# Kernel tuning notes

Hardware: AMD Instinct MI355X
Metric: run time of the kernel (lower is better)

Reference implementation:

```python
import jax, jax.numpy as jnp
import numpy as np

# Geometry constants hardcoded in the torch module
B, H, W = 1, 256, 256
A, DC = 64, 1024            # n_views, det_count
NSAMP = 512                  # samples per ray for the line integral
DSRC, DDET, SPACING = 500.0, 500.0, 2.0
NPAD = 2048                  # fft padding (next pow2 >= 2*DC)
FEAT = 32


def _bilinear_image(img, px, py):
    """Bilinear sample img (B,H,W) at centered coords px,py (any shape). Zero outside."""
    b, hh, ww = img.shape
    cx = px + (ww - 1) / 2.0
    cy = py + (hh - 1) / 2.0
    x0 = jnp.floor(cx); y0 = jnp.floor(cy)
    fx = cx - x0; fy = cy - y0
    x0i = x0.astype(jnp.int32); y0i = y0.astype(jnp.int32)
    flat = img.reshape(b, -1)

    def gather(yi, xi):
        valid = (yi >= 0) & (yi < hh) & (xi >= 0) & (xi < ww)
        yc = jnp.clip(yi, 0, hh - 1); xc = jnp.clip(xi, 0, ww - 1)
        idx = (yc * ww + xc).reshape(-1)
        v = jnp.take(flat, idx, axis=1).reshape((b,) + yi.shape)
        return v * valid.astype(img.dtype)

    return (gather(y0i, x0i) * (1 - fx) * (1 - fy)
            + gather(y0i, x0i + 1) * fx * (1 - fy)
            + gather(y0i + 1, x0i) * (1 - fx) * fy
            + gather(y0i + 1, x0i + 1) * fx * fy)


def fan_forward(img, theta):
    """Ray-driven fan-beam forward projection. img (B,1,H,W) -> sino (B,A,DC)."""
    im = img[:, 0]
    c = jnp.cos(theta); s = jnp.sin(theta)
    src = DSRC * jnp.stack([c, s], -1)                    # (A,2) source positions
    e = jnp.stack([-s, c], -1)                            # detector axis
    u = (jnp.arange(DC) - (DC - 1) / 2.0) * SPACING       # detector offsets
    det = -DDET * jnp.stack([c, s], -1)[:, None, :] + u[None, :, None] * e[:, None, :]  # (A,DC,2)
    d = det - src[:, None, :]
    L = jnp.sqrt(jnp.sum(d * d, axis=-1))                 # (A,DC) ray lengths
    t = (jnp.arange(NSAMP, dtype=jnp.float32) + 0.5) / NSAMP
    pts = src[:, None, None, :] + t[None, None, :, None] * d[:, :, None, :]  # (A,DC,N,2)
    vals = _bilinear_image(im, pts[..., 0], pts[..., 1])  # (B,A,DC,N)
    return jnp.sum(vals, axis=-1) * (L / NSAMP)[None]


def filter_sinogram(sino):
    """Ram-Lak ramp filtering along the detector axis with zero-padding."""
    f = jnp.abs(jnp.fft.rfftfreq(NPAD)).astype(jnp.float32)  # cycles/sample
    sf = jnp.fft.rfft(sino, n=NPAD, axis=-1) * (2.0 * f)
    return jnp.fft.irfft(sf, n=NPAD, axis=-1)[..., :DC].astype(sino.dtype)


def fan_backprojection(sino, theta):
    """Pixel-driven fan-beam backprojection. sino (B,A,DC) -> (B,1,H,W)."""
    xs = jnp.arange(W, dtype=jnp.float32) - (W - 1) / 2.0
    ys = jnp.arange(H, dtype=jnp.float32) - (H - 1) / 2.0
    gx, gy = jnp.meshgrid(xs, ys)                         # (H,W)
    c = jnp.cos(theta)[:, None, None]; s = jnp.sin(theta)[:, None, None]
    xr = gx[None] * c + gy[None] * s                      # (A,H,W) rotated coords
    yr = -gx[None] * s + gy[None] * c
    denom = DSRC - xr
    uu = yr * (DSRC + DDET) / denom                       # detector coordinate
    wgt = (DSRC * DSRC) / (denom * denom)                 # fan-beam distance weight
    iu = uu / SPACING + (DC - 1) / 2.0
    i0 = jnp.floor(iu); fr = iu - i0
    i0i = i0.astype(jnp.int32)
    aidx = jnp.arange(A)[:, None, None]
    b = sino.shape[0]
    flat = sino.reshape(b, -1)

    def g(ii):
        valid = (ii >= 0) & (ii < DC)
        ic = jnp.clip(ii, 0, DC - 1)
        idx = (aidx * DC + ic).reshape(-1)
        v = jnp.take(flat, idx, axis=1).reshape((b, A, H, W))
        return v * valid.astype(sino.dtype)

    vals = g(i0i) * (1 - fr) + g(i0i + 1) * fr            # (B,A,H,W)
    bp = jnp.sum(vals * wgt[None], axis=1) * (jnp.pi / A)
    return bp[:, None]


def conv(x, w):
    return jax.lax.conv_general_dilated(x, w, (1, 1), 'SAME',
                                        dimension_numbers=('NCHW', 'OIHW', 'NCHW'))


def setup_inputs():
    key = jax.random.key(0)
    ks = jax.random.split(key, 8)
    x = jax.random.normal(ks[0], (B, 1, H, W), jnp.float32)
    theta = jnp.arange(A, dtype=jnp.float32) * (2.0 * np.pi / A)
    sinogram = jax.random.normal(ks[1], (B, A, DC), jnp.float32)

    def xav(k, shape):
        fan_in = shape[1] * 9; fan_out = shape[0] * 9
        return jax.random.normal(k, shape, jnp.float32) * np.sqrt(2.0 / (fan_in + fan_out)).astype(np.float32)

    return {
        'x': x, 'theta': theta, 'sinogram': sinogram,
        'lambda_step': jnp.float32(0.5), 'soft_thr': jnp.float32(0.01),
        'conv1_forward': xav(ks[2], (FEAT, 1, 3, 3)),
        'conv2_forward': xav(ks[3], (FEAT, FEAT, 3, 3)),
        'conv1_backward': xav(ks[4], (FEAT, FEAT, 3, 3)),
        'conv2_backward': xav(ks[5], (1, FEAT, 3, 3)),
    }


def reference(x, theta, sinogram, lambda_step, soft_thr,
              conv1_forward, conv2_forward, conv1_backward, conv2_backward):
    sino_pred = fan_forward(x, theta)
    filtered = filter_sinogram(sino_pred)
    X_fbp = fan_backprojection(filtered - sinogram, theta)
    x_input = x - lambda_step * X_fbp
    h = jax.nn.relu(conv(x_input, conv1_forward))
    x_forward = conv(h, conv2_forward)
    hs = jnp.sign(x_forward) * jax.nn.relu(jnp.abs(x_forward) - soft_thr)
    x_pred = conv(jax.nn.relu(conv(hs, conv1_backward)), conv2_backward)
    x_est = conv(jax.nn.relu(conv(x_forward, conv1_backward)), conv2_backward)
    symloss = x_est - x_input
    return (x_pred, symloss)
```

## Files before the change

### kernel.cpp

```cpp
#include <hip/hip_runtime.h>

#define DEV_INLINE __device__ __forceinline__

#define PI_F 3.14159265358979323846f

#define H_OFF     0
#define SINO_OFF  2048
#define DIFF_OFF  67584
#define XIN_OFF   133120
#define WF2F_OFF  198656
#define WF1B_OFF  207872
#define WF2B_OFF  212480
#define BUFA_OFF  217088
#define BUFB_OFF  2314240

typedef short bf16x8 __attribute__((ext_vector_type(8)));
typedef float f32x4 __attribute__((ext_vector_type(4)));

union FragI4 { int4 i4; bf16x8 v; };
union FragI  { int i[4]; bf16x8 v; };

DEV_INLINE unsigned rne1(float a) {
  unsigned u = __float_as_uint(a);
  return (u + 0x7FFFu + ((u >> 16) & 1u)) >> 16;
}
DEV_INLINE int pack_rne(float a, float b) {
  return (int)(rne1(a) | (rne1(b) << 16));
}

__global__ __launch_bounds__(256) void setup_kernel(
    const float* __restrict__ sino_in, const float* __restrict__ w2f,
    const float* __restrict__ w1b, const float* __restrict__ w2b,
    const float* __restrict__ img,
    float* __restrict__ h, float* __restrict__ diff,
    int* __restrict__ wf2f, int* __restrict__ wf1b, int* __restrict__ wf2b,
    float4* __restrict__ quadP, float* __restrict__ x_input) {
  const int b = blockIdx.x;
  const int tid = threadIdx.x;
  if (b < 64) {
    __shared__ float hp[8][32];
    const int cell = tid & 31;
    const int kq = tid >> 5;
    const int n = b * 32 + cell;
    float ssum = 0.0f;
    const float ang_scale = PI_F / 1024.0f;
    for (int k = kq * 128; k < kq * 128 + 128; ++k) {
      int m = (k * n) & 2047;
      ssum += (float)k * __cosf((float)m * ang_scale);
    }
    hp[kq][cell] = ssum;
    __syncthreads();
    if (tid < 32) {
      float S = 0.0f;
      #pragma unroll
      for (int q = 0; q < 8; ++q) S += hp[q][tid];
      int nn = b * 32 + tid;
      float sgn = (nn & 1) ? -1.0f : 1.0f;
      h[nn] = (S * (1.0f / 512.0f) + sgn) * (1.0f / 2048.0f);
    }
  } else if (b < 320) {
    int idx = (b - 64) * 256 + tid;
    diff[idx] = -sino_in[idx];
  } else if (b < 356) {
    const bool second = (b >= 338);
    int idx = (b - (second ? 338 : 320)) * 256 + tid;
    int d = idx & 3;
    int L = (idx >> 2) & 63;
    int jm = idx >> 8;
    int j = jm >> 1, mt = jm & 1;
    int co = mt * 16 + (L & 15);
    int ci0 = (L >> 4) * 8 + 2 * d;
    const float* w = second ? w1b : w2f;
    int v = pack_rne(w[co * 288 + ci0 * 9 + j], w[co * 288 + (ci0 + 1) * 9 + j]);
    (second ? wf1b : wf2f)[idx] = v;
  } else if (b < 617) {
    int idx = (b - 356) * 256 + tid;
    if (idx < 258 * 258) {
      int y = idx / 258;
      int x = idx - y * 258;
      float4 v;
      int ay = y - 1, bx = x - 1;
      bool y0ok = (ay >= 0 && ay < 256);
      bool y1ok = (ay + 1 >= 0 && ay + 1 < 256);
      bool x0ok = (bx >= 0 && bx < 256);
      bool x1ok = (bx + 1 >= 0 && bx + 1 < 256);
      v.x = (y0ok && x0ok) ? img[(ay << 8) + bx] : 0.0f;
      v.y = (y0ok && x1ok) ? img[(ay << 8) + bx + 1] : 0.0f;
      v.z = (y1ok && x0ok) ? img[((ay + 1) << 8) + bx] : 0.0f;
      v.w = (y1ok && x1ok) ? img[((ay + 1) << 8) + bx + 1] : 0.0f;
      quadP[idx] = v;
    }
  } else if (b < 873) {
    int idx = (b - 617) * 256 + tid;
    x_input[idx] = img[idx];
  } else {
    int d = tid & 3;
    int L = tid >> 2;
    int n = L & 15;
    int k0 = (L >> 4) * 8 + 2 * d;
    float lo = (n < 9) ? w2b[k0 * 9 + n] : 0.0f;
    float hi = (n < 9) ? w2b[(k0 + 1) * 9 + n] : 0.0f;
    wf2b[tid] = pack_rne(lo, hi);
  }
}

__global__ __launch_bounds__(256) void fwdproj(
    const float4* __restrict__ quadP, const float* __restrict__ theta,
    float* __restrict__ sino) {
  __shared__ float part[8][32];
  __shared__ float cs[2];
  const int tid = threadIdx.x;
  const int a = blockIdx.x >> 5;
  const int cell = tid & 31;
  const int chunk = tid >> 5;
  const int d = ((blockIdx.x & 31) << 5) + cell;
  if (tid == 0) {
    float th = theta[a];
    cs[0] = cosf(th);
    cs[1] = sinf(th);
  }
  __syncthreads();
  const float c = cs[0], s = cs[1];
  const float u = ((float)d - 511.5f) * 2.0f;
  const float dxv = -1000.0f * c - u * s;
  const float dyv = -1000.0f * s + u * c;
  const float L = sqrtf(1.0e6f + u * u);
  const float sx = fmaf(500.0f, c, 127.5f);
  const float sy = fmaf(500.0f, s, 127.5f);

  float tlo = 0.0f, thi = 1.0f;
  if (fabsf(dxv) > 1e-6f) {
    float inv = 1.0f / dxv;
    float a0 = (-1.0f - sx) * inv, a1 = (256.0f - sx) * inv;
    tlo = fmaxf(tlo, fminf(a0, a1));
    thi = fminf(thi, fmaxf(a0, a1));
  } else if (sx <= -1.0f || sx >= 256.0f) {
    thi = -1.0f;
  }
  if (fabsf(dyv) > 1e-6f) {
    float inv = 1.0f / dyv;
    float a0 = (-1.0f - sy) * inv, a1 = (256.0f - sy) * inv;
    tlo = fmaxf(tlo, fminf(a0, a1));
    thi = fminf(thi, fmaxf(a0, a1));
  } else if (sy <= -1.0f || sy >= 256.0f) {
    thi = -1.0f;
  }
  int imin = (int)ceilf(tlo * 512.0f - 0.5f) - 1;
  imin = imin < 0 ? 0 : imin;
  int imax = (int)floorf(thi * 512.0f - 0.5f) + 1;
  imax = imax > 511 ? 511 : imax;

  float acc = 0.0f;
  for (int i = imin + chunk; i <= imax; i += 8) {
    float t = ((float)i + 0.5f) * (1.0f / 512.0f);
    float cx = fmaf(t, dxv, sx);
    float cy = fmaf(t, dyv, sy);
    cx = fminf(fmaxf(cx, -1.0f), 256.0f);
    cy = fminf(fmaxf(cy, -1.0f), 256.0f);
    float xf = floorf(cx), yf = floorf(cy);
    float fx = cx - xf, fy = cy - yf;
    int ix = (int)xf + 1;
    int iy = (int)yf + 1;
    float4 q = quadP[iy * 258 + ix];
    float gx = 1.0f - fx, gy = 1.0f - fy;
    acc += gy * (gx * q.x + fx * q.y) + fy * (gx * q.z + fx * q.w);
  }
  part[chunk][cell] = acc;
  __syncthreads();
  if (tid < 32) {
    float r = 0.0f;
    #pragma unroll
    for (int q = 0; q < 8; ++q) r += part[q][tid];
    sino[a * 1024 + ((blockIdx.x & 31) << 5) + tid] = r * (L * (1.0f / 512.0f));
  }
}

__global__ __launch_bounds__(256) void filt(
    const float* __restrict__ sino_pred, const float* __restrict__ h,
    float* __restrict__ diff) {
  __shared__ __align__(16) float srow[256];
  __shared__ __align__(16) float hext[4104];
  const int a = blockIdx.x >> 2;
  const int q = blockIdx.x & 3;
  const int tid = threadIdx.x;
  const int k0base = q * 256;
  srow[tid] = sino_pred[a * 1024 + k0base + tid];
  for (int n = tid; n < 4104; n += 256) hext[n] = h[(n - 2051) & 2047];
  __syncthreads();
  const int dd0 = tid * 4;
  float acc0 = 0.f, acc1 = 0.f, acc2 = 0.f, acc3 = 0.f;
  #pragma unroll 4
  for (int kk = 0; kk < 256; kk += 4) {
    float4 sv = *reinterpret_cast<const float4*>(&srow[kk]);
    int nb = dd0 + 2048 - k0base - kk;
    float4 hA = *reinterpret_cast<const float4*>(&hext[nb]);
    float4 hB = *reinterpret_cast<const float4*>(&hext[nb + 4]);
    acc0 = fmaf(sv.x, hA.w, acc0); acc0 = fmaf(sv.y, hA.z, acc0);
    acc0 = fmaf(sv.z, hA.y, acc0); acc0 = fmaf(sv.w, hA.x, acc0);
    acc1 = fmaf(sv.x, hB.x, acc1); acc1 = fmaf(sv.y, hA.w, acc1);
    acc1 = fmaf(sv.z, hA.z, acc1); acc1 = fmaf(sv.w, hA.y, acc1);
    acc2 = fmaf(sv.x, hB.y, acc2); acc2 = fmaf(sv.y, hB.x, acc2);
    acc2 = fmaf(sv.z, hA.w, acc2); acc2 = fmaf(sv.w, hA.z, acc2);
    acc3 = fmaf(sv.x, hB.z, acc3); acc3 = fmaf(sv.y, hB.y, acc3);
    acc3 = fmaf(sv.z, hB.x, acc3); acc3 = fmaf(sv.w, hA.w, acc3);
  }
  float* o = diff + a * 1024 + dd0;
  atomicAdd(o + 0, acc0);
  atomicAdd(o + 1, acc1);
  atomicAdd(o + 2, acc2);
  atomicAdd(o + 3, acc3);
}

__global__ __launch_bounds__(256) void backproj_part(
    const float* __restrict__ diff, const float* __restrict__ theta,
    const float* __restrict__ lam_p, float* __restrict__ x_input) {
  __shared__ float cst[16], snt[16];
  const int tid = threadIdx.x;
  const int tileb = blockIdx.x & 255;
  const int a0 = (blockIdx.x >> 8) << 4;
  if (tid < 16) {
    float th = theta[a0 + tid];
    cst[tid] = cosf(th);
    snt[tid] = sinf(th);
  }
  __syncthreads();
  const int tX = (tileb & 3) << 6;
  const int tY = (tileb >> 2) << 2;
  const int pxi = tX + (tid & 63);
  const int pyi = tY + (tid >> 6);
  const float gx = (float)pxi - 127.5f;
  const float gy = (float)pyi - 127.5f;
  float acc = 0.0f;
  for (int ai = 0; ai < 16; ++ai) {
    float c = cst[ai], s = snt[ai];
    float xr = gx * c + gy * s;
    float yr = gy * c - gx * s;
    float denom = 500.0f - xr;
    float inv = 1.0f / denom;
    float uu = yr * 1000.0f * inv;
    float wgt = 250000.0f * inv * inv;
    float iu = uu * 0.5f + 511.5f;
    float i0f = floorf(iu);
    float fr = iu - i0f;
    int i0 = (int)i0f;
    int c0 = min(max(i0, 0), 1023);
    int c1 = min(max(i0 + 1, 0), 1023);
    float m0 = (i0 >= 0 && i0 < 1024) ? 1.0f : 0.0f;
    float m1 = (i0 + 1 >= 0 && i0 + 1 < 1024) ? 1.0f : 0.0f;
    const float* row = diff + (a0 + ai) * 1024;
    float v0 = row[c0] * m0;
    float v1 = row[c1] * m1;
    acc += (v0 * (1.0f - fr) + v1 * fr) * wgt;
  }
  int p = (pyi << 8) + pxi;
  atomicAdd(x_input + p, -lam_p[0] * 0.04908738521234052f * acc);
}

__global__ __launch_bounds__(256) void conv12f(
    const float* __restrict__ x_input, const float* __restrict__ w1f,
    const int* __restrict__ wf2f, int* __restrict__ xfp) {
  __shared__ float xin[8][68];
  __shared__ int htile[6732];
  const int tid = threadIdx.x;
  const int lane = tid & 63;
  const int wave = tid >> 6;
  const int tX = (blockIdx.x & 3) << 6;
  const int tY = (blockIdx.x >> 2) << 2;

  FragI4 wf[2][9];
  const int4* wfg = (const int4*)wf2f;
  #pragma unroll
  for (int mt = 0; mt < 2; ++mt)
    #pragma unroll
    for (int j = 0; j < 9; ++j) wf[mt][j].i4 = wfg[(j * 2 + mt) * 64 + lane];

  for (int idx = tid; idx < 544; idx += 256) {
    int sy = idx / 68;
    int sx = idx - sy * 68;
    int gy = tY + sy - 2, gx = tX + sx - 2;
    xin[sy][sx] = (gy >= 0 && gy < 256 && gx >= 0 && gx < 256)
                      ? x_input[(gy << 8) + gx] : 0.0f;
  }
  __syncthreads();

  for (int pos = tid; pos < 396; pos += 256) {
    int yy = pos / 66;
    int xx = pos - yy * 66;
    int hy = tY + yy - 1, hx = tX + xx - 1;
    bool hin = (hy >= 0 && hy < 256 && hx >= 0 && hx < 256);
    float v[9];
    #pragma unroll
    for (int dy = 0; dy < 3; ++dy)
      #pragma unroll
      for (int dx = 0; dx < 3; ++dx) v[dy * 3 + dx] = xin[yy + dy][xx + dx];
    #pragma unroll
    for (int c2 = 0; c2 < 16; ++c2) {
      float r0 = 0.0f, r1 = 0.0f;
      #pragma unroll
      for (int j = 0; j < 9; ++j) {
        r0 = fmaf(v[j], w1f[(2 * c2) * 9 + j], r0);
        r1 = fmaf(v[j], w1f[(2 * c2 + 1) * 9 + j], r1);
      }
      r0 = hin ? fmaxf(r0, 0.0f) : 0.0f;
      r1 = hin ? fmaxf(r1, 0.0f) : 0.0f;
      htile[pos * 17 + c2] = pack_rne(r0, r1);
    }
  }
  __syncthreads();

  const int y = wave;
  const int n = lane & 15;
  const int q = lane >> 4;
  for (int xt = 0; xt < 4; ++xt) {
    const int x0 = xt << 4;
    f32x4 acc0 = {0.f, 0.f, 0.f, 0.f};
    f32x4 acc1 = {0.f, 0.f, 0.f, 0.f};
    #pragma unroll
    for (int j = 0; j < 9; ++j) {
      int dy = j / 3, dx = j - dy * 3;
      int pb = (y + dy) * 66 + x0 + dx;
      int base = (pb + n) * 17 + q * 4;
      FragI bf;
      bf.i[0] = htile[base];
      bf.i[1] = htile[base + 1];
      bf.i[2] = htile[base + 2];
      bf.i[3] = htile[base + 3];
      acc0 = __builtin_amdgcn_mfma_f32_16x16x32_bf16(wf[0][j].v, bf.v, acc0, 0, 0, 0);
      acc1 = __builtin_amdgcn_mfma_f32_16x16x32_bf16(wf[1][j].v, bf.v, acc1, 0, 0, 0);
    }
    const int gpos = ((tY + y) << 8) + tX + x0 + n;
    xfp[((q * 2) << 16) + gpos]         = pack_rne(acc0[0], acc0[1]);
    xfp[((q * 2 + 1) << 16) + gpos]     = pack_rne(acc0[2], acc0[3]);
    xfp[((8 + q * 2) << 16) + gpos]     = pack_rne(acc1[0], acc1[1]);
    xfp[((8 + q * 2 + 1) << 16) + gpos] = pack_rne(acc1[2], acc1[3]);
  }
}

__global__ __launch_bounds__(256) void branch_tail(
    const int* __restrict__ xfp, const int* __restrict__ wf1b,
    const int* __restrict__ wf2b, const float* __restrict__ thr_p,
    const float* __restrict__ x_input, float* __restrict__ out) {
  __shared__ int ldsX[9248];
  __shared__ int ldsD[6800];
  float* ldsP = (float*)ldsX;
  const int tid = threadIdx.x;
  const int lane = tid & 63;
  const int wave = tid >> 6;
  const int branch = blockIdx.x >> 8;
  const int tileb = blockIdx.x & 255;
  const int tX = (tileb & 3) << 6;
  const int tY = (tileb >> 2) << 2;
  const float thr = thr_p[0];
  const bool soft = (branch == 0);

  FragI4 wf[2][9];
  const int4* wfg = (const int4*)wf1b;
  #pragma unroll
  for (int mt = 0; mt < 2; ++mt)
    #pragma unroll
    for (int j = 0; j < 9; ++j) wf[mt][j].i4 = wfg[(j * 2 + mt) * 64 + lane];
  FragI4 wb;
  wb.i4 = ((const int4*)wf2b)[lane];

  int pp[3], ga[3];
  bool ok[3];
  #pragma unroll
  for (int t = 0; t < 3; ++t) {
    int p = tid + t * 256;
    pp[t] = p;
    int sy = p / 68;
    int sx = p - sy * 68;
    int gy = tY + sy - 2, gx = tX + sx - 2;
    ok[t] = (p < 544) && ((unsigned)gy < 256u) && ((unsigned)gx < 256u);
    ga[t] = (gy << 8) + gx;
  }
  #pragma unroll
  for (int c2 = 0; c2 < 16; ++c2) {
    #pragma unroll
    for (int t = 0; t < 3; ++t) {
      if (pp[t] < 544) {
        int v = ok[t] ? xfp[(c2 << 16) + ga[t]] : 0;
        if (soft) {
          float lo = __uint_as_float(((unsigned)v) << 16);
          float hi = __uint_as_float(((unsigned)v) & 0xFFFF0000u);
          lo = fmaxf(lo - thr, 0.0f) + fminf(lo + thr, 0.0f);
          hi = fmaxf(hi - thr, 0.0f) + fminf(hi + thr, 0.0f);
          v = pack_rne(lo, hi);
        }
        ldsX[pp[t] * 17 + c2] = v;
      }
    }
  }
  __syncthreads();

  const int n = lane & 15;
  const int q = lane >> 4;
  const int rxtab[5] = {-1, 15, 31, 47, 49};
  for (int t = wave; t < 30; t += 4) {
    int trow = t / 5;
    int ry = trow - 1;
    int rx0 = rxtab[t - trow * 5];
    int rxn = rx0 + n;
    bool inimg = ((unsigned)(tX + rxn) < 256u) && ((unsigned)(tY + ry) < 256u);
    int wrbase = ((ry + 1) * 66 + rxn + 1) * 17;
    f32x4 acc0 = {0.f, 0.f, 0.f, 0.f};
    f32x4 acc1 = {0.f, 0.f, 0.f, 0.f};
    #pragma unroll
    for (int j = 0; j < 9; ++j) {
      int dy = j / 3, dx = j - dy * 3;
      int pb = (ry + 1 + dy) * 68 + rx0 + 1 + dx;
      int base = (pb + n) * 17 + q * 4;
      FragI bf;
      bf.i[0] = ldsX[base];
      bf.i[1] = ldsX[base + 1];
      bf.i[2] = ldsX[base + 2];
      bf.i[3] = ldsX[base + 3];
      acc0 = __builtin_amdgcn_mfma_f32_16x16x32_bf16(wf[0][j].v, bf.v, acc0, 0, 0, 0);
      acc1 = __builtin_amdgcn_mfma_f32_16x16x32_bf16(wf[1][j].v, bf.v, acc1, 0, 0, 0);
    }
    float a00 = inimg ? fmaxf(acc0[0], 0.0f) : 0.0f;
    float a01 = inimg ? fmaxf(acc0[1], 0.0f) : 0.0f;
    float a02 = inimg ? fmaxf(acc0[2], 0.0f) : 0.0f;
    float a03 = inimg ? fmaxf(acc0[3], 0.0f) : 0.0f;
    float a10 = inimg ? fmaxf(acc1[0], 0.0f) : 0.0f;
    float a11 = inimg ? fmaxf(acc1[1], 0.0f) : 0.0f;
    float a12 = inimg ? fmaxf(acc1[2], 0.0f) : 0.0f;
    float a13 = inimg ? fmaxf(acc1[3], 0.0f) : 0.0f;
    ldsD[wrbase + q * 2]         = pack_rne(a00, a01);
    ldsD[wrbase + q * 2 + 1]     = pack_rne(a02, a03);
    ldsD[wrbase + 8 + q * 2]     = pack_rne(a10, a11);
    ldsD[wrbase + 8 + q * 2 + 1] = pack_rne(a12, a13);
  }
  __syncthreads();

  for (int t = wave; t < 25; t += 4) {
    int pbase = t << 4;
    int abase = (pbase + n) * 17 + q * 4;
    FragI af;
    af.i[0] = ldsD[abase];
    af.i[1] = ldsD[abase + 1];
    af.i[2] = ldsD[abase + 2];
    af.i[3] = ldsD[abase + 3];
    f32x4 acc = {0.f, 0.f, 0.f, 0.f};
    acc = __builtin_amdgcn_mfma_f32_16x16x32_bf16(af.v, wb.v, acc, 0, 0, 0);
    #pragma unroll
    for (int r = 0; r < 4; ++r)
      ldsP[(pbase + q * 4 + r) * 17 + n] = acc[r];
  }
  __syncthreads();

  const int px = tid & 63, py = tid >> 6;
  float acc = 0.0f;
  #pragma unroll
  for (int j = 0; j < 9; ++j) {
    int dy = j / 3, dx = j - dy * 3;
    int rp = (py + dy) * 66 + px + dx;
    acc += ldsP[rp * 17 + j];
  }
  const int p = ((tY + py) << 8) + tX + px;
  if (branch == 0) out[p] = acc;
  else out[65536 + p] = acc - x_input[p];
}

extern "C" void kernel_launch(void* const* d_in, const int* in_sizes, int n_in,
                              void* d_out, int out_size, void* d_ws, size_t ws_size,
                              hipStream_t stream) {
  const float* x       = (const float*)d_in[0];
  const float* theta   = (const float*)d_in[1];
  const float* sino_in = (const float*)d_in[2];
  const float* lam     = (const float*)d_in[3];
  const float* thr     = (const float*)d_in[4];
  const float* w_c1f   = (const float*)d_in[5];
  const float* w_c2f   = (const float*)d_in[6];
  const float* w_c1b   = (const float*)d_in[7];
  const float* w_c2b   = (const float*)d_in[8];
  float* out = (float*)d_out;
  float* ws  = (float*)d_ws;

  float* h         = ws + H_OFF;
  float* sino_pred = ws + SINO_OFF;
  float* diff      = ws + DIFF_OFF;
  float* x_input   = ws + XIN_OFF;
  int*   wf2f      = (int*)(ws + WF2F_OFF);
  int*   wf1b      = (int*)(ws + WF1B_OFF);
  int*   wf2b      = (int*)(ws + WF2B_OFF);
  float4* quadP    = (float4*)(ws + BUFA_OFF);
  int*   xfp       = (int*)(ws + BUFB_OFF);

  setup_kernel<<<874, 256, 0, stream>>>(sino_in, w_c2f, w_c1b, w_c2b, x, h,
                                        diff, wf2f, wf1b, wf2b, quadP, x_input);
  fwdproj<<<2048, 256, 0, stream>>>(quadP, theta, sino_pred);
  filt<<<256, 256, 0, stream>>>(sino_pred, h, diff);
  backproj_part<<<1024, 256, 0, stream>>>(diff, theta, lam, x_input);
  conv12f<<<256, 256, 0, stream>>>(x_input, w_c1f, wf2f, xfp);
  branch_tail<<<512, 256, 0, stream>>>(xfp, wf1b, wf2b, thr, x_input, out);
}
```

Baseline: 143.2 us.

## Filter whole sinogram rows per block and retile branch_tail to 32x8

The ramp filter now computes each view's full convolution in one block with direct stores that subtract the measured sinogram. This removes the atomics and the setup pass that initialised diff to the negated input. The branch_tail kernel moves from 64x4 to 32x8 output tiles, which shrinks the halo LDS footprint and may raise occupancy. The cost is that the filter now runs only 64 blocks, each with a four times longer loop, so GPU utilisation in that stage drops.

```diff
diff --git a/kernel.cpp b/kernel.cpp
--- a/kernel.cpp
+++ b/kernel.cpp
@@ -29,12 +29,11 @@
 }
 
 __global__ __launch_bounds__(256) void setup_kernel(
-    const float* __restrict__ sino_in, const float* __restrict__ w2f,
-    const float* __restrict__ w1b, const float* __restrict__ w2b,
-    const float* __restrict__ img,
-    float* __restrict__ h, float* __restrict__ diff,
-    int* __restrict__ wf2f, int* __restrict__ wf1b, int* __restrict__ wf2b,
-    float4* __restrict__ quadP, float* __restrict__ x_input) {
+    const float* __restrict__ w2f, const float* __restrict__ w1b,
+    const float* __restrict__ w2b, const float* __restrict__ img,
+    float* __restrict__ h, int* __restrict__ wf2f, int* __restrict__ wf1b,
+    int* __restrict__ wf2b, float4* __restrict__ quadP,
+    float* __restrict__ x_input) {
   const int b = blockIdx.x;
   const int tid = threadIdx.x;
   if (b < 64) {
@@ -58,12 +57,9 @@
       float sgn = (nn & 1) ? -1.0f : 1.0f;
       h[nn] = (S * (1.0f / 512.0f) + sgn) * (1.0f / 2048.0f);
     }
-  } else if (b < 320) {
-    int idx = (b - 64) * 256 + tid;
-    diff[idx] = -sino_in[idx];
-  } else if (b < 356) {
-    const bool second = (b >= 338);
-    int idx = (b - (second ? 338 : 320)) * 256 + tid;
+  } else if (b < 100) {
+    const bool second = (b >= 82);
+    int idx = (b - (second ? 82 : 64)) * 256 + tid;
     int d = idx & 3;
     int L = (idx >> 2) & 63;
     int jm = idx >> 8;
@@ -73,8 +69,16 @@
     const float* w = second ? w1b : w2f;
     int v = pack_rne(w[co * 288 + ci0 * 9 + j], w[co * 288 + (ci0 + 1) * 9 + j]);
     (second ? wf1b : wf2f)[idx] = v;
-  } else if (b < 617) {
-    int idx = (b - 356) * 256 + tid;
+  } else if (b < 101) {
+    int d = tid & 3;
+    int L = tid >> 2;
+    int n = L & 15;
+    int k0 = (L >> 4) * 8 + 2 * d;
+    float lo = (n < 9) ? w2b[k0 * 9 + n] : 0.0f;
+    float hi = (n < 9) ? w2b[(k0 + 1) * 9 + n] : 0.0f;
+    wf2b[tid] = pack_rne(lo, hi);
+  } else if (b < 362) {
+    int idx = (b - 101) * 256 + tid;
     if (idx < 258 * 258) {
       int y = idx / 258;
       int x = idx - y * 258;
@@ -90,17 +94,9 @@
       v.w = (y1ok && x1ok) ? img[((ay + 1) << 8) + bx + 1] : 0.0f;
       quadP[idx] = v;
     }
-  } else if (b < 873) {
-    int idx = (b - 617) * 256 + tid;
+  } else {
+    int idx = (b - 362) * 256 + tid;
     x_input[idx] = img[idx];
-  } else {
-    int d = tid & 3;
-    int L = tid >> 2;
-    int n = L & 15;
-    int k0 = (L >> 4) * 8 + 2 * d;
-    float lo = (n < 9) ? w2b[k0 * 9 + n] : 0.0f;
-    float hi = (n < 9) ? w2b[(k0 + 1) * 9 + n] : 0.0f;
-    wf2b[tid] = pack_rne(lo, hi);
   }
 }
 
@@ -175,24 +171,22 @@
   }
 }
 
-__global__ __launch_bounds__(256) void filt(
+__global__ __launch_bounds__(256) void filt64(
     const float* __restrict__ sino_pred, const float* __restrict__ h,
-    float* __restrict__ diff) {
-  __shared__ __align__(16) float srow[256];
+    const float* __restrict__ sino_in, float* __restrict__ diff) {
+  __shared__ __align__(16) float srow[1024];
   __shared__ __align__(16) float hext[4104];
-  const int a = blockIdx.x >> 2;
-  const int q = blockIdx.x & 3;
-  const int tid = threadIdx.x;
-  const int k0base = q * 256;
-  srow[tid] = sino_pred[a * 1024 + k0base + tid];
+  const int a = blockIdx.x;
+  const int tid = threadIdx.x;
+  for (int n = tid; n < 1024; n += 256) srow[n] = sino_pred[a * 1024 + n];
   for (int n = tid; n < 4104; n += 256) hext[n] = h[(n - 2051) & 2047];
   __syncthreads();
   const int dd0 = tid * 4;
   float acc0 = 0.f, acc1 = 0.f, acc2 = 0.f, acc3 = 0.f;
   #pragma unroll 4
-  for (int kk = 0; kk < 256; kk += 4) {
+  for (int kk = 0; kk < 1024; kk += 4) {
     float4 sv = *reinterpret_cast<const float4*>(&srow[kk]);
-    int nb = dd0 + 2048 - k0base - kk;
+    int nb = dd0 + 2048 - kk;
     float4 hA = *reinterpret_cast<const float4*>(&hext[nb]);
     float4 hB = *reinterpret_cast<const float4*>(&hext[nb + 4]);
     acc0 = fmaf(sv.x, hA.w, acc0); acc0 = fmaf(sv.y, hA.z, acc0);
@@ -204,11 +198,12 @@
     acc3 = fmaf(sv.x, hB.z, acc3); acc3 = fmaf(sv.y, hB.y, acc3);
     acc3 = fmaf(sv.z, hB.x, acc3); acc3 = fmaf(sv.w, hA.w, acc3);
   }
+  const float4 sref = *reinterpret_cast<const float4*>(&sino_in[a * 1024 + dd0]);
   float* o = diff + a * 1024 + dd0;
-  atomicAdd(o + 0, acc0);
-  atomicAdd(o + 1, acc1);
-  atomicAdd(o + 2, acc2);
-  atomicAdd(o + 3, acc3);
+  o[0] = acc0 - sref.x;
+  o[1] = acc1 - sref.y;
+  o[2] = acc2 - sref.z;
+  o[3] = acc3 - sref.w;
 }
 
 __global__ __launch_bounds__(256) void backproj_part(
@@ -340,16 +335,16 @@
     const int* __restrict__ xfp, const int* __restrict__ wf1b,
     const int* __restrict__ wf2b, const float* __restrict__ thr_p,
     const float* __restrict__ x_input, float* __restrict__ out) {
-  __shared__ int ldsX[9248];
-  __shared__ int ldsD[6800];
+  __shared__ int ldsX[7344];
+  __shared__ int ldsD[5984];
   float* ldsP = (float*)ldsX;
   const int tid = threadIdx.x;
   const int lane = tid & 63;
   const int wave = tid >> 6;
   const int branch = blockIdx.x >> 8;
   const int tileb = blockIdx.x & 255;
-  const int tX = (tileb & 3) << 6;
-  const int tY = (tileb >> 2) << 2;
+  const int tX = (tileb & 7) << 5;
+  const int tY = (tileb >> 3) << 3;
   const float thr = thr_p[0];
   const bool soft = (branch == 0);
 
@@ -362,23 +357,23 @@
   FragI4 wb;
   wb.i4 = ((const int4*)wf2b)[lane];
 
-  int pp[3], ga[3];
-  bool ok[3];
+  int pp[2], ga[2];
+  bool ok[2];
   #pragma unroll
-  for (int t = 0; t < 3; ++t) {
+  for (int t = 0; t < 2; ++t) {
     int p = tid + t * 256;
     pp[t] = p;
-    int sy = p / 68;
-    int sx = p - sy * 68;
+    int sy = p / 36;
+    int sx = p - sy * 36;
     int gy = tY + sy - 2, gx = tX + sx - 2;
-    ok[t] = (p < 544) && ((unsigned)gy < 256u) && ((unsigned)gx < 256u);
+    ok[t] = (p < 432) && ((unsigned)gy < 256u) && ((unsigned)gx < 256u);
     ga[t] = (gy << 8) + gx;
   }
   #pragma unroll
   for (int c2 = 0; c2 < 16; ++c2) {
     #pragma unroll
-    for (int t = 0; t < 3; ++t) {
-      if (pp[t] < 544) {
+    for (int t = 0; t < 2; ++t) {
+      if (pp[t] < 432) {
         int v = ok[t] ? xfp[(c2 << 16) + ga[t]] : 0;
         if (soft) {
           float lo = __uint_as_float(((unsigned)v) << 16);
@@ -395,20 +390,20 @@
 
   const int n = lane & 15;
   const int q = lane >> 4;
-  const int rxtab[5] = {-1, 15, 31, 47, 49};
+  const int rx0tab[3] = {-1, 15, 17};
   for (int t = wave; t < 30; t += 4) {
-    int trow = t / 5;
+    int trow = t / 3;
     int ry = trow - 1;
-    int rx0 = rxtab[t - trow * 5];
+    int rx0 = rx0tab[t - trow * 3];
     int rxn = rx0 + n;
     bool inimg = ((unsigned)(tX + rxn) < 256u) && ((unsigned)(tY + ry) < 256u);
-    int wrbase = ((ry + 1) * 66 + rxn + 1) * 17;
+    int wrbase = ((ry + 1) * 34 + rxn + 1) * 17;
     f32x4 acc0 = {0.f, 0.f, 0.f, 0.f};
     f32x4 acc1 = {0.f, 0.f, 0.f, 0.f};
     #pragma unroll
     for (int j = 0; j < 9; ++j) {
       int dy = j / 3, dx = j - dy * 3;
-      int pb = (ry + 1 + dy) * 68 + rx0 + 1 + dx;
+      int pb = (ry + 1 + dy) * 36 + rx0 + 1 + dx;
       int base = (pb + n) * 17 + q * 4;
       FragI bf;
       bf.i[0] = ldsX[base];
@@ -433,7 +428,7 @@
   }
   __syncthreads();
 
-  for (int t = wave; t < 25; t += 4) {
+  for (int t = wave; t < 22; t += 4) {
     int pbase = t << 4;
     int abase = (pbase + n) * 17 + q * 4;
     FragI af;
@@ -449,12 +444,12 @@
   }
   __syncthreads();
 
-  const int px = tid & 63, py = tid >> 6;
+  const int px = tid & 31, py = tid >> 5;
   float acc = 0.0f;
   #pragma unroll
   for (int j = 0; j < 9; ++j) {
     int dy = j / 3, dx = j - dy * 3;
-    int rp = (py + dy) * 66 + px + dx;
+    int rp = (py + dy) * 34 + px + dx;
     acc += ldsP[rp * 17 + j];
   }
   const int p = ((tY + py) << 8) + tX + px;
@@ -487,10 +482,10 @@
   float4* quadP    = (float4*)(ws + BUFA_OFF);
   int*   xfp       = (int*)(ws + BUFB_OFF);
 
-  setup_kernel<<<874, 256, 0, stream>>>(sino_in, w_c2f, w_c1b, w_c2b, x, h,
-                                        diff, wf2f, wf1b, wf2b, quadP, x_input);
+  setup_kernel<<<618, 256, 0, stream>>>(w_c2f, w_c1b, w_c2b, x, h, wf2f,
+                                        wf1b, wf2b, quadP, x_input);
   fwdproj<<<2048, 256, 0, stream>>>(quadP, theta, sino_pred);
-  filt<<<256, 256, 0, stream>>>(sino_pred, h, diff);
+  filt64<<<64, 256, 0, stream>>>(sino_pred, h, sino_in, diff);
   backproj_part<<<1024, 256, 0, stream>>>(diff, theta, lam, x_input);
   conv12f<<<256, 256, 0, stream>>>(x_input, w_c1f, wf2f, xfp);
   branch_tail<<<512, 256, 0, stream>>>(xfp, wf1b, wf2b, thr, x_input, out);
```

New measurement: 155.7 us. 8.7% more time.
